# Kernel tuning notes

Hardware: AMD Instinct MI355X
Metric: run time of the kernel (lower is better)

The kernel has to match this reference:

```python
import jax, jax.numpy as jnp
import numpy as np

BLOCK_LEN = 64


def segsum(x):
    """x: (..., T) -> (..., T, T) with segsum[i,j] = sum_{k=j+1..i} x[k] (lower-tri incl diag), -inf above."""
    T = x.shape[-1]
    xc = jnp.cumsum(x, axis=-1)
    seg = xc[..., :, None] - xc[..., None, :]
    mask = jnp.tril(jnp.ones((T, T), dtype=bool))
    return jnp.where(mask, seg, -jnp.inf)


def setup_inputs() -> dict:
    key = jax.random.key(0)
    kx, ka, kb, kc = jax.random.split(key, 4)
    b, s, h, p, n = 4, 4096, 32, 64, 64
    X = jax.random.normal(kx, (b, s, h), dtype=jnp.float32)  # placeholder to keep split order stable
    X = jax.random.normal(kx, (b, s, h, p), dtype=jnp.float32)
    # A must be negative for a stable SSM decay (exp of cumulative sums stays bounded)
    A = -jax.random.uniform(ka, (b, s, h), dtype=jnp.float32, minval=0.0, maxval=1.0)
    B = jax.random.normal(kb, (b, s, h, n), dtype=jnp.float32)
    C = jax.random.normal(kc, (b, s, h, n), dtype=jnp.float32)
    return {"X": X, "A": A, "B": B, "C": C}


def reference(X, A, B, C):
    blk = BLOCK_LEN
    b, s, h, p = X.shape
    n = B.shape[-1]
    c = s // blk
    # chunk: b (c l) ... -> b c l ...
    Xc = X.reshape(b, c, blk, h, p)
    Bc = B.reshape(b, c, blk, h, n)
    Cc = C.reshape(b, c, blk, h, n)
    Ac = A.reshape(b, c, blk, h).transpose(0, 3, 1, 2)  # b h c l
    A_cumsum = jnp.cumsum(Ac, axis=-1)                  # b h c l

    # 1. intra-chunk (diagonal block) output
    L = jnp.exp(segsum(Ac))                             # b h c l s
    Y_diag = jnp.einsum("bclhn,bcshn,bhcls,bcshp->bclhp", Cc, Bc, L, Xc)

    # 2. intra-chunk states (chunk-final state assuming zero initial state)
    decay_states = jnp.exp(A_cumsum[..., -1:] - A_cumsum)
    states = jnp.einsum("bclhn,bhcl,bclhp->bchpn", Bc, decay_states, Xc)

    # 3. inter-chunk recurrence over chunk boundaries
    init = jnp.zeros_like(states[:, :1])
    states = jnp.concatenate([init, states], axis=1)    # b (c+1) h p n
    A_last = jnp.pad(A_cumsum[..., -1], ((0, 0), (0, 0), (1, 0)))  # b h (c+1)
    decay_chunk = jnp.exp(segsum(A_last))               # b h (c+1) (c+1)
    new_states = jnp.einsum("bhzc,bchpn->bzhpn", decay_chunk, states)
    states_in = new_states[:, :-1]                      # state entering each chunk

    # 4. state -> output
    state_decay_out = jnp.exp(A_cumsum)
    Y_off = jnp.einsum("bclhn,bchpn,bhcl->bclhp", Cc, states_in, state_decay_out)

    Y = (Y_diag + Y_off).reshape(b, s, h, p)
    return Y
```

## Files before the change

### kernel.cpp

```cpp
#include <hip/hip_runtime.h>

namespace {

typedef __attribute__((ext_vector_type(8))) short short8;
typedef __attribute__((ext_vector_type(4))) float f32x4;

constexpr int Hh = 32, Ssq = 4096, NCH = 64;
constexpr int GR = 2048;
constexpr int ST = 68;

__device__ inline unsigned short f2bf(float f) {
  unsigned u = __float_as_uint(f);
  u += 0x7FFFu + ((u >> 16) & 1u);
  return (unsigned short)(u >> 16);
}
__device__ inline float bf2f(unsigned short s) {
  return __uint_as_float(((unsigned)s) << 16);
}

__device__ inline short8 frag(const unsigned short* p) {
  union { short8 s; uint2 u[2]; } r;
  r.u[0] = *(const uint2*)p;
  r.u[1] = *(const uint2*)(p + 4);
  return r.s;
}

__global__ __launch_bounds__(256, 8)
void k1a_chunkstate(const float* __restrict__ X0, const float* __restrict__ A0,
                    const float* __restrict__ B0, unsigned short* __restrict__ S16) {
  __shared__ unsigned short BTs[64 * ST];
  __shared__ unsigned short XTs[64 * ST];
  __shared__ float ielb[64];
  __shared__ float eab;

  const int tid = threadIdx.x;
  const int hi = blockIdx.x & 31, ci = (blockIdx.x >> 5) & 63, bi = blockIdx.x >> 11;
  if (ci == 63) return;

  const float* Xg = X0 + (((size_t)bi * Ssq + ci * 64) * Hh + hi) * 64;
  const float* Bg = B0 + (((size_t)bi * Ssq + ci * 64) * Hh + hi) * 64;
  const float* Ag = A0 + ((size_t)bi * Ssq + ci * 64) * Hh + hi;
  unsigned short* sp = S16 + ((size_t)(bi * Hh + hi) * NCH + ci) * 4096;

  const int w = tid >> 6, lane = tid & 63, lr = lane & 15, lk = lane >> 4;

  if (tid < 64) {
    float a = Ag[(size_t)tid * Hh];
#pragma unroll
    for (int off = 1; off < 64; off <<= 1) {
      float v = __shfl_up(a, off);
      if (tid >= off) a += v;
    }
    ielb[tid] = __expf(-a);
    if (tid == 63) eab = __expf(a);
  }
  __syncthreads();

  {
    const int r = tid >> 2, cb = (tid & 3) * 4;
    const float iel = ielb[r];
    const float* bp = Bg + (size_t)r * GR;
    const float* xp = Xg + (size_t)r * GR;
#pragma unroll
    for (int j = 0; j < 4; ++j) {
      const int c = cb + 16 * j;
      float4 bv = *(const float4*)(bp + c);
      BTs[(c + 0) * ST + r] = f2bf(bv.x * iel);
      BTs[(c + 1) * ST + r] = f2bf(bv.y * iel);
      BTs[(c + 2) * ST + r] = f2bf(bv.z * iel);
      BTs[(c + 3) * ST + r] = f2bf(bv.w * iel);
      float4 xv = *(const float4*)(xp + c);
      XTs[(c + 0) * ST + r] = f2bf(xv.x);
      XTs[(c + 1) * ST + r] = f2bf(xv.y);
      XTs[(c + 2) * ST + r] = f2bf(xv.z);
      XTs[(c + 3) * ST + r] = f2bf(xv.w);
    }
  }
  __syncthreads();

  const float ea = eab;
#pragma unroll
  for (int tp = 0; tp < 4; ++tp) {
    f32x4 acc = {0.f, 0.f, 0.f, 0.f};
#pragma unroll
    for (int ks = 0; ks < 2; ++ks)
      acc = __builtin_amdgcn_mfma_f32_16x16x32_bf16(
          frag(&XTs[(tp * 16 + lr) * ST + ks * 32 + lk * 8]),
          frag(&BTs[(w * 16 + lr) * ST + ks * 32 + lk * 8]), acc, 0, 0, 0);
#pragma unroll
    for (int i = 0; i < 4; ++i)
      sp[(tp * 16 + lk * 4 + i) * 64 + w * 16 + lr] = f2bf(acc[i] * ea);
  }
}

__global__ __launch_bounds__(256)
void k1b_scan(const float* __restrict__ A0, unsigned short* __restrict__ S16) {
  __shared__ float part[256];
  __shared__ float eat[64];

  const int tid = threadIdx.x;
  const int sl8 = blockIdx.x & 7, hi = (blockIdx.x >> 3) & 31, bi = blockIdx.x >> 8;
  const float* Ag = A0 + (size_t)bi * Ssq * Hh + hi;

  {
    const int c = tid >> 2, q = tid & 3;
    float s = 0.f;
#pragma unroll
    for (int k = 0; k < 16; ++k) s += Ag[(size_t)(c * 64 + q * 16 + k) * Hh];
    part[tid] = s;
  }
  __syncthreads();
  if (tid < 64)
    eat[tid] = __expf(part[tid * 4] + part[tid * 4 + 1] + part[tid * 4 + 2] + part[tid * 4 + 3]);
  __syncthreads();

  unsigned short* base =
      S16 + (size_t)(bi * Hh + hi) * NCH * 4096 + sl8 * 512 + tid * 2;
  float s0 = 0.f, s1 = 0.f;

  auto L = [&](int c) -> unsigned {
    return (c < 63) ? *(const unsigned*)(base + (size_t)c * 4096) : 0u;
  };
  auto step = [&](int c, unsigned v) {
    const float ea = eat[c];
    s0 = s0 * ea + bf2f((unsigned short)(v & 0xffffu));
    s1 = s1 * ea + bf2f((unsigned short)(v >> 16));
    *(unsigned*)(base + (size_t)(c + 1) * 4096) =
        (unsigned)f2bf(s0) | ((unsigned)f2bf(s1) << 16);
  };

  unsigned q0 = L(0), q1 = L(1), q2 = L(2), q3 = L(3);
  for (int c = 0; c < 60; c += 4) {
    step(c + 0, q0); q0 = L(c + 4);
    step(c + 1, q1); q1 = L(c + 5);
    step(c + 2, q2); q2 = L(c + 6);
    step(c + 3, q3); q3 = L(c + 7);
  }
  step(60, q0); step(61, q1); step(62, q2);
}

__global__ __launch_bounds__(256, 4)
void k2_y(const float* __restrict__ X0, const float* __restrict__ A0,
          const float* __restrict__ B0, const float* __restrict__ C0,
          const unsigned short* __restrict__ S16, float* __restrict__ Y0) {
  __shared__ unsigned short Cs[64 * ST];
  __shared__ unsigned short Bsh[64 * ST];
  __shared__ unsigned short XT[64 * ST];
  __shared__ unsigned short Sb[64 * ST];
  __shared__ float elb[64], ielb2[64];

  const int tid = threadIdx.x;
  const int hi = blockIdx.x & 31, ci = (blockIdx.x >> 5) & 63, bi = blockIdx.x >> 11;

  const float* Xg = X0 + (((size_t)bi * Ssq + ci * 64) * Hh + hi) * 64;
  const float* Bg = B0 + (((size_t)bi * Ssq + ci * 64) * Hh + hi) * 64;
  const float* Cg = C0 + (((size_t)bi * Ssq + ci * 64) * Hh + hi) * 64;
  const float* Ag = A0 + ((size_t)bi * Ssq + ci * 64) * Hh + hi;
  const unsigned short* Sg = S16 + ((size_t)(bi * Hh + hi) * NCH + ci) * 4096;
  float* Yg = Y0 + (((size_t)bi * Ssq + ci * 64) * Hh + hi) * 64;

  const int w = tid >> 6, lane = tid & 63, lr = lane & 15, lk = lane >> 4;

  if (tid < 64) {
    float a = Ag[(size_t)tid * Hh];
#pragma unroll
    for (int off = 1; off < 64; off <<= 1) {
      float v = __shfl_up(a, off);
      if (tid >= off) a += v;
    }
    elb[tid] = __expf(a);
    ielb2[tid] = __expf(-a);
  }
  __syncthreads();

  {
    const int r = tid >> 2, cb = (tid & 3) * 4;
    const float iel = ielb2[r];
    const float* bp = Bg + (size_t)r * GR;
    const float* cp = Cg + (size_t)r * GR;
    const float* xp = Xg + (size_t)r * GR;
#pragma unroll
    for (int j = 0; j < 4; ++j) {
      const int c = cb + 16 * j;
      float4 bv = *(const float4*)(bp + c);
      float4 cv = *(const float4*)(cp + c);
      unsigned short bb[4] = {f2bf(bv.x * iel), f2bf(bv.y * iel),
                              f2bf(bv.z * iel), f2bf(bv.w * iel)};
      unsigned short cc[4] = {f2bf(cv.x), f2bf(cv.y), f2bf(cv.z), f2bf(cv.w)};
      *(uint2*)&Bsh[r * ST + c] = *(const uint2*)bb;
      *(uint2*)&Cs[r * ST + c] = *(const uint2*)cc;
      float4 xv = *(const float4*)(xp + c);
      XT[(c + 0) * ST + r] = f2bf(xv.x);
      XT[(c + 1) * ST + r] = f2bf(xv.y);
      XT[(c + 2) * ST + r] = f2bf(xv.z);
      XT[(c + 3) * ST + r] = f2bf(xv.w);
    }
    if (ci == 0) {
#pragma unroll
      for (int j = 0; j < 4; ++j) {
        const int q = tid + j * 256;
        uint2 z = {0u, 0u};
        *(uint2*)&Sb[(q >> 4) * ST + (q & 15) * 4] = z;
      }
    } else {
#pragma unroll
      for (int j = 0; j < 4; ++j) {
        const int q = tid + j * 256;
        *(uint2*)&Sb[(q >> 4) * ST + (q & 15) * 4] = *(const uint2*)(Sg + q * 4);
      }
    }
  }
  __syncthreads();

  int tl[3] = {-1, -1, -1}, ts[3] = {0, 0, 0};
  int zr[2] = {-1, -1}, zc[2] = {0, 0};
  switch (w) {
    case 0: tl[0] = 0; ts[0] = 0; tl[1] = 1; ts[1] = 0; tl[2] = 1; ts[2] = 1;
            zr[0] = 0; zc[0] = 1; zr[1] = 0; zc[1] = 2; break;
    case 1: tl[0] = 2; ts[0] = 0; tl[1] = 2; ts[1] = 1; tl[2] = 2; ts[2] = 2;
            zr[0] = 0; zc[0] = 3; break;
    case 2: tl[0] = 3; ts[0] = 0; tl[1] = 3; ts[1] = 1;
            zr[0] = 1; zc[0] = 2; zr[1] = 1; zc[1] = 3; break;
    case 3: tl[0] = 3; ts[0] = 2; tl[1] = 3; ts[1] = 3;
            zr[0] = 2; zc[0] = 3; break;
  }
  f32x4 ga[3];
#pragma unroll
  for (int t = 0; t < 3; ++t) {
    ga[t] = (f32x4){0.f, 0.f, 0.f, 0.f};
    if (tl[t] >= 0) {
#pragma unroll
      for (int ks = 0; ks < 2; ++ks)
        ga[t] = __builtin_amdgcn_mfma_f32_16x16x32_bf16(
            frag(&Cs[(tl[t] * 16 + lr) * ST + ks * 32 + lk * 8]),
            frag(&Bsh[(ts[t] * 16 + lr) * ST + ks * 32 + lk * 8]), ga[t], 0, 0, 0);
    }
  }
  __syncthreads();

  {
#pragma unroll
    for (int t = 0; t < 3; ++t) {
      if (tl[t] >= 0) {
        const int gcol = ts[t] * 16 + lr;
#pragma unroll
        for (int i = 0; i < 4; ++i) {
          const int grow = tl[t] * 16 + lk * 4 + i;
          float gv = (gcol <= grow) ? ga[t][i] * elb[grow] : 0.f;
          Bsh[grow * ST + gcol] = f2bf(gv);
        }
      }
    }
    const int zrow = lane >> 2, zq = lane & 3;
    uint2 z = {0u, 0u};
#pragma unroll
    for (int t = 0; t < 2; ++t)
      if (zr[t] >= 0)
        *(uint2*)&Bsh[(zr[t] * 16 + zrow) * ST + zc[t] * 16 + zq * 4] = z;
  }
  __syncthreads();

  {
#pragma unroll
    for (int tp = 0; tp < 4; ++tp) {
      f32x4 aD = {0.f, 0.f, 0.f, 0.f}, aO = {0.f, 0.f, 0.f, 0.f};
#pragma unroll
      for (int ks = 0; ks < 2; ++ks) {
        const int ko = ks * 32 + lk * 8;
        aD = __builtin_amdgcn_mfma_f32_16x16x32_bf16(
            frag(&Bsh[(w * 16 + lr) * ST + ko]), frag(&XT[(tp * 16 + lr) * ST + ko]), aD, 0, 0, 0);
        aO = __builtin_amdgcn_mfma_f32_16x16x32_bf16(
            frag(&Cs[(w * 16 + lr) * ST + ko]), frag(&Sb[(tp * 16 + lr) * ST + ko]), aO, 0, 0, 0);
      }
#pragma unroll
      for (int i = 0; i < 4; ++i) {
        const int row = w * 16 + lk * 4 + i;
        Yg[(size_t)row * GR + tp * 16 + lr] = aD[i] + elb[row] * aO[i];
      }
    }
  }
}

}

extern "C" void kernel_launch(void* const* d_in, const int* in_sizes, int n_in,
                              void* d_out, int out_size, void* d_ws, size_t ws_size,
                              hipStream_t stream) {
  const float* X = (const float*)d_in[0];
  const float* A = (const float*)d_in[1];
  const float* B = (const float*)d_in[2];
  const float* C = (const float*)d_in[3];
  float* Y = (float*)d_out;
  unsigned short* S16 = (unsigned short*)d_ws;
  (void)in_sizes; (void)n_in; (void)out_size; (void)ws_size;
  k1a_chunkstate<<<dim3(8192), dim3(256), 0, stream>>>(X, A, B, S16);
  k1b_scan<<<dim3(1024), dim3(256), 0, stream>>>(A, S16);
  k2_y<<<dim3(8192), dim3(256), 0, stream>>>(X, A, B, C, S16, Y);
}
```

Before: 241.4 us.

## Switch chunk GEMMs to 32x32x16 MFMA and read states directly from global

Replaces the 16x16x32 bf16 MFMA tiling with 32x32x16 tiles (one 32x32 output tile per wave) in both the chunk-state and output kernels, using 128-bit LDS fragment loads with a padded stride of 72. The output kernel no longer stages the inter-chunk state in LDS; each wave loads its state fragments straight from global memory, and the off-diagonal MFMA is skipped for the first chunk. Dropping that shared buffer lowers LDS usage and allows raising launch bounds to 5 blocks per CU. The intent is fewer MFMA issues and fragment loads, less LDS traffic, and higher occupancy, at the cost of uncoalesced global fragment loads and fewer concurrent tiles per wave.

```diff
diff --git a/kernel.cpp b/kernel.cpp
--- a/kernel.cpp
+++ b/kernel.cpp
@@ -3,11 +3,11 @@
 namespace {
 
 typedef __attribute__((ext_vector_type(8))) short short8;
-typedef __attribute__((ext_vector_type(4))) float f32x4;
+typedef __attribute__((ext_vector_type(16))) float f32x16;
 
 constexpr int Hh = 32, Ssq = 4096, NCH = 64;
 constexpr int GR = 2048;
-constexpr int ST = 68;
+constexpr int ST = 72;
 
 __device__ inline unsigned short f2bf(float f) {
   unsigned u = __float_as_uint(f);
@@ -18,18 +18,15 @@
   return __uint_as_float(((unsigned)s) << 16);
 }
 
-__device__ inline short8 frag(const unsigned short* p) {
-  union { short8 s; uint2 u[2]; } r;
-  r.u[0] = *(const uint2*)p;
-  r.u[1] = *(const uint2*)(p + 4);
-  return r.s;
+__device__ inline short8 frag128(const unsigned short* base, int row, int ks, int lhi) {
+  return *(const short8*)(base + row * ST + ks * 16 + lhi * 8);
 }
 
 __global__ __launch_bounds__(256, 8)
 void k1a_chunkstate(const float* __restrict__ X0, const float* __restrict__ A0,
                     const float* __restrict__ B0, unsigned short* __restrict__ S16) {
-  __shared__ unsigned short BTs[64 * ST];
-  __shared__ unsigned short XTs[64 * ST];
+  __shared__ __align__(16) unsigned short BTs[64 * ST];
+  __shared__ __align__(16) unsigned short XTs[64 * ST];
   __shared__ float ielb[64];
   __shared__ float eab;
 
@@ -42,7 +39,8 @@
   const float* Ag = A0 + ((size_t)bi * Ssq + ci * 64) * Hh + hi;
   unsigned short* sp = S16 + ((size_t)(bi * Hh + hi) * NCH + ci) * 4096;
 
-  const int w = tid >> 6, lane = tid & 63, lr = lane & 15, lk = lane >> 4;
+  const int w = tid >> 6, lane = tid & 63;
+  const int l31 = lane & 31, lhi = lane >> 5;
 
   if (tid < 64) {
     float a = Ag[(size_t)tid * Hh];
@@ -78,18 +76,19 @@
   }
   __syncthreads();
 
+  const int tp = w >> 1, tn = w & 1;
+  f32x16 acc = {};
+#pragma unroll
+  for (int ks = 0; ks < 4; ++ks)
+    acc = __builtin_amdgcn_mfma_f32_32x32x16_bf16(
+        frag128(XTs, 32 * tp + l31, ks, lhi),
+        frag128(BTs, 32 * tn + l31, ks, lhi),
+        acc, 0, 0, 0);
   const float ea = eab;
 #pragma unroll
-  for (int tp = 0; tp < 4; ++tp) {
-    f32x4 acc = {0.f, 0.f, 0.f, 0.f};
-#pragma unroll
-    for (int ks = 0; ks < 2; ++ks)
-      acc = __builtin_amdgcn_mfma_f32_16x16x32_bf16(
-          frag(&XTs[(tp * 16 + lr) * ST + ks * 32 + lk * 8]),
-          frag(&BTs[(w * 16 + lr) * ST + ks * 32 + lk * 8]), acc, 0, 0, 0);
-#pragma unroll
-    for (int i = 0; i < 4; ++i)
-      sp[(tp * 16 + lk * 4 + i) * 64 + w * 16 + lr] = f2bf(acc[i] * ea);
+  for (int i = 0; i < 16; ++i) {
+    const int p = 32 * tp + (i & 3) + 8 * (i >> 2) + 4 * lhi;
+    sp[p * 64 + 32 * tn + l31] = f2bf(acc[i] * ea);
   }
 }
 
@@ -139,14 +138,13 @@
   step(60, q0); step(61, q1); step(62, q2);
 }
 
-__global__ __launch_bounds__(256, 4)
+__global__ __launch_bounds__(256, 5)
 void k2_y(const float* __restrict__ X0, const float* __restrict__ A0,
           const float* __restrict__ B0, const float* __restrict__ C0,
           const unsigned short* __restrict__ S16, float* __restrict__ Y0) {
-  __shared__ unsigned short Cs[64 * ST];
-  __shared__ unsigned short Bsh[64 * ST];
-  __shared__ unsigned short XT[64 * ST];
-  __shared__ unsigned short Sb[64 * ST];
+  __shared__ __align__(16) unsigned short Cs[64 * ST];
+  __shared__ __align__(16) unsigned short Bsh[64 * ST];
+  __shared__ __align__(16) unsigned short XT[64 * ST];
   __shared__ float elb[64], ielb2[64];
 
   const int tid = threadIdx.x;
@@ -159,7 +157,8 @@
   const unsigned short* Sg = S16 + ((size_t)(bi * Hh + hi) * NCH + ci) * 4096;
   float* Yg = Y0 + (((size_t)bi * Ssq + ci * 64) * Hh + hi) * 64;
 
-  const int w = tid >> 6, lane = tid & 63, lr = lane & 15, lk = lane >> 4;
+  const int w = tid >> 6, lane = tid & 63;
+  const int l31 = lane & 31, lhi = lane >> 5;
 
   if (tid < 64) {
     float a = Ag[(size_t)tid * Hh];
@@ -195,88 +194,65 @@
       XT[(c + 2) * ST + r] = f2bf(xv.z);
       XT[(c + 3) * ST + r] = f2bf(xv.w);
     }
-    if (ci == 0) {
-#pragma unroll
-      for (int j = 0; j < 4; ++j) {
-        const int q = tid + j * 256;
-        uint2 z = {0u, 0u};
-        *(uint2*)&Sb[(q >> 4) * ST + (q & 15) * 4] = z;
-      }
-    } else {
-#pragma unroll
-      for (int j = 0; j < 4; ++j) {
-        const int q = tid + j * 256;
-        *(uint2*)&Sb[(q >> 4) * ST + (q & 15) * 4] = *(const uint2*)(Sg + q * 4);
-      }
-    }
-  }
-  __syncthreads();
-
-  int tl[3] = {-1, -1, -1}, ts[3] = {0, 0, 0};
-  int zr[2] = {-1, -1}, zc[2] = {0, 0};
-  switch (w) {
-    case 0: tl[0] = 0; ts[0] = 0; tl[1] = 1; ts[1] = 0; tl[2] = 1; ts[2] = 1;
-            zr[0] = 0; zc[0] = 1; zr[1] = 0; zc[1] = 2; break;
-    case 1: tl[0] = 2; ts[0] = 0; tl[1] = 2; ts[1] = 1; tl[2] = 2; ts[2] = 2;
-            zr[0] = 0; zc[0] = 3; break;
-    case 2: tl[0] = 3; ts[0] = 0; tl[1] = 3; ts[1] = 1;
-            zr[0] = 1; zc[0] = 2; zr[1] = 1; zc[1] = 3; break;
-    case 3: tl[0] = 3; ts[0] = 2; tl[1] = 3; ts[1] = 3;
-            zr[0] = 2; zc[0] = 3; break;
-  }
-  f32x4 ga[3];
-#pragma unroll
-  for (int t = 0; t < 3; ++t) {
-    ga[t] = (f32x4){0.f, 0.f, 0.f, 0.f};
-    if (tl[t] >= 0) {
-#pragma unroll
-      for (int ks = 0; ks < 2; ++ks)
-        ga[t] = __builtin_amdgcn_mfma_f32_16x16x32_bf16(
-            frag(&Cs[(tl[t] * 16 + lr) * ST + ks * 32 + lk * 8]),
-            frag(&Bsh[(ts[t] * 16 + lr) * ST + ks * 32 + lk * 8]), ga[t], 0, 0, 0);
-    }
-  }
-  __syncthreads();
-
-  {
-#pragma unroll
-    for (int t = 0; t < 3; ++t) {
-      if (tl[t] >= 0) {
-        const int gcol = ts[t] * 16 + lr;
-#pragma unroll
-        for (int i = 0; i < 4; ++i) {
-          const int grow = tl[t] * 16 + lk * 4 + i;
-          float gv = (gcol <= grow) ? ga[t][i] * elb[grow] : 0.f;
-          Bsh[grow * ST + gcol] = f2bf(gv);
-        }
-      }
-    }
-    const int zrow = lane >> 2, zq = lane & 3;
-    uint2 z = {0u, 0u};
-#pragma unroll
-    for (int t = 0; t < 2; ++t)
-      if (zr[t] >= 0)
-        *(uint2*)&Bsh[(zr[t] * 16 + zrow) * ST + zc[t] * 16 + zq * 4] = z;
-  }
-  __syncthreads();
-
-  {
-#pragma unroll
-    for (int tp = 0; tp < 4; ++tp) {
-      f32x4 aD = {0.f, 0.f, 0.f, 0.f}, aO = {0.f, 0.f, 0.f, 0.f};
-#pragma unroll
-      for (int ks = 0; ks < 2; ++ks) {
-        const int ko = ks * 32 + lk * 8;
-        aD = __builtin_amdgcn_mfma_f32_16x16x32_bf16(
-            frag(&Bsh[(w * 16 + lr) * ST + ko]), frag(&XT[(tp * 16 + lr) * ST + ko]), aD, 0, 0, 0);
-        aO = __builtin_amdgcn_mfma_f32_16x16x32_bf16(
-            frag(&Cs[(w * 16 + lr) * ST + ko]), frag(&Sb[(tp * 16 + lr) * ST + ko]), aO, 0, 0, 0);
-      }
-#pragma unroll
-      for (int i = 0; i < 4; ++i) {
-        const int row = w * 16 + lk * 4 + i;
-        Yg[(size_t)row * GR + tp * 16 + lr] = aD[i] + elb[row] * aO[i];
-      }
+  }
+  __syncthreads();
+
+  const int ati = (w == 0) ? 0 : 1;
+  const int atj = (w == 2) ? 1 : 0;
+  f32x16 ga = {};
+  if (w < 3) {
+#pragma unroll
+    for (int ks = 0; ks < 4; ++ks)
+      ga = __builtin_amdgcn_mfma_f32_32x32x16_bf16(
+          frag128(Cs, 32 * ati + l31, ks, lhi),
+          frag128(Bsh, 32 * atj + l31, ks, lhi),
+          ga, 0, 0, 0);
+  }
+  __syncthreads();
+
+  if (w < 3) {
+    const int gcol = 32 * atj + l31;
+#pragma unroll
+    for (int i = 0; i < 16; ++i) {
+      const int grow = 32 * ati + (i & 3) + 8 * (i >> 2) + 4 * lhi;
+      float gv = (gcol <= grow) ? ga[i] * elb[grow] : 0.f;
+      Bsh[grow * ST + gcol] = f2bf(gv);
+    }
+  } else {
+    const short8 z8 = {};
+    *(short8*)&Bsh[l31 * ST + 32 + lhi * 16] = z8;
+    *(short8*)&Bsh[l31 * ST + 40 + lhi * 16] = z8;
+  }
+  __syncthreads();
+
+  {
+    const int ti = w >> 1, tj = w & 1;
+    short8 sf[4];
+    if (ci != 0) {
+      const unsigned short* srow = Sg + (32 * tj + l31) * 64;
+#pragma unroll
+      for (int ks = 0; ks < 4; ++ks)
+        sf[ks] = *(const short8*)(srow + ks * 16 + lhi * 8);
+    }
+    f32x16 aD = {}, aO = {};
+#pragma unroll
+    for (int ks = 0; ks < 4; ++ks)
+      aD = __builtin_amdgcn_mfma_f32_32x32x16_bf16(
+          frag128(Bsh, 32 * ti + l31, ks, lhi),
+          frag128(XT, 32 * tj + l31, ks, lhi),
+          aD, 0, 0, 0);
+    if (ci != 0) {
+#pragma unroll
+      for (int ks = 0; ks < 4; ++ks)
+        aO = __builtin_amdgcn_mfma_f32_32x32x16_bf16(
+            frag128(Cs, 32 * ti + l31, ks, lhi),
+            sf[ks],
+            aO, 0, 0, 0);
+    }
+#pragma unroll
+    for (int i = 0; i < 16; ++i) {
+      const int row = 32 * ti + (i & 3) + 8 * (i >> 2) + 4 * lhi;
+      Yg[(size_t)row * GR + 32 * tj + l31] = aD[i] + elb[row] * aO[i];
     }
   }
 }
```

After: 240.8 us. About the same (-0.2%).
